# Optimization experiments

Hardware: AMD Instinct MI355X
Metric: run time of the kernel (lower is better)

## Reference

```python
import jax, jax.numpy as jnp
import numpy as np

EPS = 1e-6
N_HEAD = 16

def alibi_slopes(n_head):
    # standard ALiBi geometric slopes for power-of-2 head counts
    start = 2.0 ** (-8.0 / n_head)
    return (start ** np.arange(1, n_head + 1)).astype(np.float32)

def rsig(x):
    # rational sigmoid sigma(x) = 0.5 * (x / (|x| + 1) + 1)
    return 0.5 * (x / (jnp.abs(x) + 1.0) + 1.0)

def mr_norm(x, w):
    # RationalMR: x / (mean(|x|) + eps) * weight
    return x / (jnp.mean(jnp.abs(x), axis=-1, keepdims=True) + EPS) * w


def setup_inputs() -> dict:
    key = jax.random.key(0)
    ks = jax.random.split(key, 6)
    d_model, d_ffn = 1024, 4096
    B, T = 1, 2048
    x = jax.random.normal(ks[0], (B, T, d_model), dtype=jnp.float32)
    s = 0.02
    w_qkv = jax.random.normal(ks[1], (3 * d_model, d_model), dtype=jnp.float32) * s
    w_out = jax.random.normal(ks[2], (d_model, d_model), dtype=jnp.float32) * s
    w_merged = jax.random.normal(ks[3], (2 * d_ffn, d_model), dtype=jnp.float32) * s
    w3 = jax.random.normal(ks[4], (d_model, d_ffn), dtype=jnp.float32) * s
    norm1_w = jnp.ones((d_model,), dtype=jnp.float32)
    norm2_w = jnp.ones((d_model,), dtype=jnp.float32)
    return {"x": x, "w_qkv": w_qkv, "w_out": w_out, "w_merged": w_merged,
            "w3": w3, "norm1_w": norm1_w, "norm2_w": norm2_w}


def reference(x, w_qkv, w_out, w_merged, w3, norm1_w, norm2_w):
    B, T, C = x.shape
    H = N_HEAD
    D = C // H
    scale = 1.0 / jnp.sqrt(jnp.float32(D))

    # --- attention sub-block ---
    h = mr_norm(x, norm1_w)
    qkv = (h @ w_qkv.T).reshape(B, T, 3, H, D).transpose(2, 0, 3, 1, 4)  # [3,B,H,T,D]
    q, k, v = qkv[0], qkv[1], qkv[2]
    scores = jnp.einsum('bhtd,bhsd->bhts', q, k) * scale  # [B,H,T,T]
    pos = jnp.arange(T)
    rel = jnp.abs(pos[:, None] - pos[None, :]).astype(jnp.float32)
    slopes = jnp.asarray(alibi_slopes(H))
    scores = scores - rel[None, None] * slopes[None, :, None, None]
    causal = pos[None, :] > pos[:, None]  # mask j > i
    scores = jnp.where(causal[None, None], jnp.float32(-10000.0), scores)
    # rational softmax: sigma(s)^4 / (sum sigma(s)^4 + eps)
    p4 = rsig(scores) ** 4
    probs = p4 / (jnp.sum(p4, axis=-1, keepdims=True) + EPS)
    attn = jnp.einsum('bhts,bhsd->bhtd', probs, v)  # [B,H,T,D]
    attn = attn.transpose(0, 2, 1, 3).reshape(B, T, C)
    x = x + attn @ w_out.T

    # --- FFN sub-block (rational SwiGLU) ---
    h2 = mr_norm(x, norm2_w)
    merged = h2 @ w_merged.T
    gate, val = jnp.split(merged, 2, axis=-1)
    hidden = gate * rsig(gate) * val
    x = x + hidden @ w3.T
    return x
```

## Files before the change

### kernel.cpp

```cpp
#include <hip/hip_runtime.h>
#include <hip/hip_bf16.h>
#include <stdint.h>

typedef unsigned int u32;
typedef unsigned short u16;
typedef __attribute__((ext_vector_type(8))) short bf16x8;
typedef __attribute__((ext_vector_type(4))) float f32x4;

#define MFMA(a, b, c) __builtin_amdgcn_mfma_f32_16x16x32_bf16(a, b, c, 0, 0, 0)

__device__ __forceinline__ u16 f2bf(float f) {
  u32 u = __float_as_uint(f);
  return (u16)((u + 0x7FFFu + ((u >> 16) & 1u)) >> 16);
}
__device__ __forceinline__ float bf2f(u16 h) {
  return __uint_as_float(((u32)h) << 16);
}
__device__ __forceinline__ float rsig_fast(float sc) {
  return 0.5f + 0.5f * sc * __builtin_amdgcn_rcpf(fabsf(sc) + 1.f);
}
__device__ __forceinline__ void async16(void* lds, const void* g) {
  __builtin_amdgcn_global_load_lds((const __attribute__((address_space(1))) u32*)g,
                                   (__attribute__((address_space(3))) u32*)lds, 16, 0, 0);
}

__global__ __launch_bounds__(256) void to_bf16_all(const float* __restrict__ s0, u16* __restrict__ d0,
                                                   const float* __restrict__ s1, u16* __restrict__ d1,
                                                   const float* __restrict__ s2, u16* __restrict__ d2,
                                                   const float* __restrict__ s3, u16* __restrict__ d3) {
  int b = blockIdx.x;
  const float* src; u16* dst;
  if (b < 1536)      { src = s0; dst = d0; }
  else if (b < 2048) { src = s1; dst = d1; b -= 1536; }
  else if (b < 6144) { src = s2; dst = d2; b -= 2048; }
  else               { src = s3; dst = d3; b -= 6144; }
  const size_t i = (size_t)b * 256 + threadIdx.x;
  const float4 a = ((const float4*)src)[2 * i];
  const float4 c = ((const float4*)src)[2 * i + 1];
  ushort4 o0, o1;
  o0.x = f2bf(a.x); o0.y = f2bf(a.y); o0.z = f2bf(a.z); o0.w = f2bf(a.w);
  o1.x = f2bf(c.x); o1.y = f2bf(c.y); o1.z = f2bf(c.z); o1.w = f2bf(c.w);
  ((ushort4*)dst)[2 * i] = o0;
  ((ushort4*)dst)[2 * i + 1] = o1;
}

__global__ __launch_bounds__(256) void mrnorm(const float* __restrict__ x,
                                              const float* __restrict__ wg,
                                              u16* __restrict__ out) {
  const int row = blockIdx.x;
  const int tid = threadIdx.x;
  const float4 v = ((const float4*)(x + (size_t)row * 1024))[tid];
  float s = fabsf(v.x) + fabsf(v.y) + fabsf(v.z) + fabsf(v.w);
#pragma unroll
  for (int off = 1; off < 64; off <<= 1) s += __shfl_xor(s, off);
  __shared__ float red[4];
  if ((tid & 63) == 0) red[tid >> 6] = s;
  __syncthreads();
  const float inv = 1.f / ((red[0] + red[1] + red[2] + red[3]) * (1.f / 1024.f) + 1e-6f);
  const float4 g = ((const float4*)wg)[tid];
  ushort4 o;
  o.x = f2bf(v.x * inv * g.x);
  o.y = f2bf(v.y * inv * g.y);
  o.z = f2bf(v.z * inv * g.z);
  o.w = f2bf(v.w * inv * g.w);
  ((ushort4*)out)[(size_t)row * 256 + tid] = o;
}

__global__ __launch_bounds__(256) void wout_reduce_norm(const u16* __restrict__ part,
                                                        const float* __restrict__ x,
                                                        const float* __restrict__ wg,
                                                        float* __restrict__ x1,
                                                        u16* __restrict__ h2) {
  const int row = blockIdx.x;
  const int tid = threadIdx.x;
  const size_t base = (size_t)row * 1024 + tid * 4;
  float4 a = *(const float4*)(x + base);
#pragma unroll
  for (int c = 0; c < 4; ++c) {
    const ushort4 p = *(const ushort4*)(part + (size_t)c * 2097152 + base);
    a.x += bf2f(p.x); a.y += bf2f(p.y); a.z += bf2f(p.z); a.w += bf2f(p.w);
  }
  *(float4*)(x1 + base) = a;
  float s = fabsf(a.x) + fabsf(a.y) + fabsf(a.z) + fabsf(a.w);
#pragma unroll
  for (int off = 1; off < 64; off <<= 1) s += __shfl_xor(s, off);
  __shared__ float red[4];
  if ((tid & 63) == 0) red[tid >> 6] = s;
  __syncthreads();
  const float inv = 1.f / ((red[0] + red[1] + red[2] + red[3]) * (1.f / 1024.f) + 1e-6f);
  const float4 g = ((const float4*)wg)[tid];
  ushort4 o;
  o.x = f2bf(a.x * inv * g.x);
  o.y = f2bf(a.y * inv * g.y);
  o.z = f2bf(a.z * inv * g.z);
  o.w = f2bf(a.w * inv * g.w);
  ((ushort4*)h2)[(size_t)row * 256 + tid] = o;
}

template <int EPI, bool DBUF>
__global__ __launch_bounds__(256) void gemm_bt(const u16* __restrict__ A, int lda,
                                               const u16* __restrict__ B, int ldb,
                                               void* __restrict__ C,
                                               const float* __restrict__ resid,
                                               int M, int N, int K) {
  __shared__ __align__(16) u16 As[(DBUF ? 2 : 1) * 128 * 64];
  __shared__ __align__(16) u16 Bs[(DBUF ? 2 : 1) * 128 * 64];
  const int tid = threadIdx.x;
  const int lane = tid & 63;
  const int w = tid >> 6;
  const int wr = (w >> 1) << 6;
  const int wc = (w & 1) << 6;
  const int nbn = N >> 7;
  const int m0 = (blockIdx.x / nbn) << 7;
  const int n0 = (blockIdx.x % nbn) << 7;
  const int l15 = lane & 15;
  const int lhi = lane >> 4;
  A += (size_t)blockIdx.y * K;
  B += (size_t)blockIdx.y * K;

  f32x4 acc[4][4] = {};

  auto stage = [&](int buf, int k0) {
#pragma unroll
    for (int p = 0; p < 4; ++p) {
      const int c = p * 256 + tid;
      const int row = c >> 3;
      const int cb = (c & 7) << 4;
      const int src = cb ^ ((row & 7) << 4);
      async16((char*)As + buf * 16384 + c * 16,
              (const char*)A + ((size_t)(m0 + row) * lda + k0) * 2 + src);
      async16((char*)Bs + buf * 16384 + c * 16,
              (const char*)B + ((size_t)(n0 + row) * ldb + k0) * 2 + src);
    }
  };
  auto compute = [&](int buf) {
#pragma unroll
    for (int kk = 0; kk < 2; ++kk) {
      bf16x8 af[4], bfr[4];
#pragma unroll
      for (int m = 0; m < 4; ++m) {
        const int row = wr + (m << 4) + l15;
        const int off = row * 128 + (((kk << 6) + (lhi << 4)) ^ ((row & 7) << 4));
        af[m] = *(const bf16x8*)((const char*)As + buf * 16384 + off);
      }
#pragma unroll
      for (int n = 0; n < 4; ++n) {
        const int row = wc + (n << 4) + l15;
        const int off = row * 128 + (((kk << 6) + (lhi << 4)) ^ ((row & 7) << 4));
        bfr[n] = *(const bf16x8*)((const char*)Bs + buf * 16384 + off);
      }
#pragma unroll
      for (int m = 0; m < 4; ++m)
#pragma unroll
        for (int n = 0; n < 4; ++n)
          acc[m][n] = MFMA(af[m], bfr[n], acc[m][n]);
    }
  };

  if (DBUF) {
    stage(0, 0);
    __syncthreads();
    int cur = 0;
    for (int k0 = 0; k0 < K; k0 += 64) {
      if (k0 + 64 < K) stage(cur ^ 1, k0 + 64);
      compute(cur);
      __syncthreads();
      cur ^= 1;
    }
  } else {
    for (int k0 = 0; k0 < K; k0 += 64) {
      stage(0, k0);
      __syncthreads();
      compute(0);
      __syncthreads();
    }
  }

  u16* Cp = (u16*)C + (size_t)blockIdx.y * M * N;
#pragma unroll
  for (int m = 0; m < 4; ++m) {
#pragma unroll
    for (int n = 0; n < 4; ++n) {
      const int col = n0 + wc + (n << 4) + l15;
#pragma unroll
      for (int r = 0; r < 4; ++r) {
        const int row = m0 + wr + (m << 4) + (lhi << 2) + r;
        const float v = acc[m][n][r];
        if (EPI == 0) {
          Cp[(size_t)row * N + col] = f2bf(v);
        } else {
          const size_t idx = (size_t)row * N + col;
          ((float*)C)[idx] = resid[idx] + v;
        }
      }
    }
  }
}

__global__ __launch_bounds__(256) void gemm_ffn1(const u16* __restrict__ A,
                                                 const u16* __restrict__ B,
                                                 u16* __restrict__ hid) {
  __shared__ __align__(16) u16 As[2][128 * 64];
  __shared__ __align__(16) u16 Bg[2][64 * 64];
  __shared__ __align__(16) u16 Bv[2][64 * 64];
  const int tid = threadIdx.x;
  const int lane = tid & 63;
  const int w = tid >> 6;
  const int wr = (w >> 1) << 6;
  const int wc = (w & 1) << 5;
  const int m0 = (blockIdx.x >> 6) << 7;
  const int n0 = (blockIdx.x & 63) << 6;
  const int l15 = lane & 15;
  const int lhi = lane >> 4;

  f32x4 ag[4][2] = {};
  f32x4 av[4][2] = {};

  auto stage = [&](int buf, int k0) {
#pragma unroll
    for (int p = 0; p < 4; ++p) {
      const int c = p * 256 + tid;
      const int row = c >> 3;
      const int cb = (c & 7) << 4;
      const int src = cb ^ ((row & 7) << 4);
      async16((char*)As[buf] + c * 16,
              (const char*)A + ((size_t)(m0 + row) * 1024 + k0) * 2 + src);
    }
#pragma unroll
    for (int p = 0; p < 2; ++p) {
      const int c = p * 256 + tid;
      const int row = c >> 3;
      const int cb = (c & 7) << 4;
      const int src = cb ^ ((row & 7) << 4);
      async16((char*)Bg[buf] + c * 16,
              (const char*)B + ((size_t)(n0 + row) * 1024 + k0) * 2 + src);
      async16((char*)Bv[buf] + c * 16,
              (const char*)B + ((size_t)(4096 + n0 + row) * 1024 + k0) * 2 + src);
    }
  };
  auto compute = [&](int buf) {
#pragma unroll
    for (int kk = 0; kk < 2; ++kk) {
      bf16x8 af[4], bgf[2], bvf[2];
#pragma unroll
      for (int m = 0; m < 4; ++m) {
        const int row = wr + (m << 4) + l15;
        const int off = row * 128 + (((kk << 6) + (lhi << 4)) ^ ((row & 7) << 4));
        af[m] = *(const bf16x8*)((const char*)As[buf] + off);
      }
#pragma unroll
      for (int n = 0; n < 2; ++n) {
        const int row = wc + (n << 4) + l15;
        const int off = row * 128 + (((kk << 6) + (lhi << 4)) ^ ((row & 7) << 4));
        bgf[n] = *(const bf16x8*)((const char*)Bg[buf] + off);
        bvf[n] = *(const bf16x8*)((const char*)Bv[buf] + off);
      }
#pragma unroll
      for (int m = 0; m < 4; ++m)
#pragma unroll
        for (int n = 0; n < 2; ++n) {
          ag[m][n] = MFMA(af[m], bgf[n], ag[m][n]);
          av[m][n] = MFMA(af[m], bvf[n], av[m][n]);
        }
    }
  };

  stage(0, 0);
  __syncthreads();
  int cur = 0;
  for (int k0 = 0; k0 < 1024; k0 += 64) {
    if (k0 + 64 < 1024) stage(cur ^ 1, k0 + 64);
    compute(cur);
    __syncthreads();
    cur ^= 1;
  }

#pragma unroll
  for (int m = 0; m < 4; ++m) {
#pragma unroll
    for (int n = 0; n < 2; ++n) {
      const int col = n0 + wc + (n << 4) + l15;
#pragma unroll
      for (int r = 0; r < 4; ++r) {
        const int row = m0 + wr + (m << 4) + (lhi << 2) + r;
        const float g = ag[m][n][r];
        const float v = av[m][n][r];
        hid[(size_t)row * 4096 + col] = f2bf(g * rsig_fast(g) * v);
      }
    }
  }
}

template <int NC, bool BF16OUT>
__global__ __launch_bounds__(256) void splitk_reduce(const u16* __restrict__ part,
                                                     size_t cstride,
                                                     const float* __restrict__ resid,
                                                     void* __restrict__ out) {
  const size_t i = ((size_t)blockIdx.x * 256 + threadIdx.x) * 8;
  float acc[8];
  if constexpr (BF16OUT) {
#pragma unroll
    for (int j = 0; j < 8; ++j) acc[j] = 0.f;
  } else {
    const float4 r0 = *(const float4*)(resid + i);
    const float4 r1 = *(const float4*)(resid + i + 4);
    acc[0] = r0.x; acc[1] = r0.y; acc[2] = r0.z; acc[3] = r0.w;
    acc[4] = r1.x; acc[5] = r1.y; acc[6] = r1.z; acc[7] = r1.w;
  }
#pragma unroll
  for (int c = 0; c < NC; ++c) {
    const uint4 p = *(const uint4*)(part + (size_t)c * cstride + i);
    const u16* ps = (const u16*)&p;
#pragma unroll
    for (int j = 0; j < 8; ++j) acc[j] += bf2f(ps[j]);
  }
  if constexpr (BF16OUT) {
    u16 ob[8];
#pragma unroll
    for (int j = 0; j < 8; ++j) ob[j] = f2bf(acc[j]);
    *(uint4*)((u16*)out + i) = *(const uint4*)ob;
  } else {
    float4 o0 = {acc[0], acc[1], acc[2], acc[3]};
    float4 o1 = {acc[4], acc[5], acc[6], acc[7]};
    *(float4*)((float*)out + i) = o0;
    *(float4*)((float*)out + i + 4) = o1;
  }
}

__global__ __launch_bounds__(256) void transpose_v(const u16* __restrict__ qkv,
                                                   u16* __restrict__ vt) {
  __shared__ __align__(16) u16 tile[64][72];
  const int head = blockIdx.x >> 5;
  const int t0 = (blockIdx.x & 31) << 6;
  const int tid = threadIdx.x;
  const int row = tid >> 2;
  const int cb = (tid & 3) << 4;
  const u16* src = qkv + (size_t)(t0 + row) * 3072 + 2048 + head * 64 + cb;
  *(uint4*)&tile[row][cb] = *(const uint4*)src;
  *(uint4*)&tile[row][cb + 8] = *(const uint4*)(src + 8);
  __syncthreads();
  u16 buf[16];
#pragma unroll
  for (int j = 0; j < 16; ++j) buf[j] = tile[cb + j][row];
  u16* dst = vt + (size_t)(head * 64 + row) * 2048 + t0 + cb;
  *(uint4*)dst = *(const uint4*)&buf[0];
  *(uint4*)(dst + 8) = *(const uint4*)&buf[8];
}

__global__ __launch_bounds__(512) void attn_part(const u16* __restrict__ qkv,
                                                 const u16* __restrict__ vt,
                                                 u16* __restrict__ pnum,
                                                 float* __restrict__ pden) {
  const int id = blockIdx.x;
  const int head = id & 15;
  const int rem = id >> 4;
  int qb2, c;
  if (rem < 4)       { qb2 = 4 + rem;                          c = 0; }
  else if (rem < 12) { const int t = rem - 4;  qb2 = 8 + (t >> 1);  c = t & 1; }
  else if (rem < 24) { const int t = rem - 12; qb2 = 12 + t / 3;    c = t % 3; }
  else               { const int t = rem - 24; qb2 = ((t & 3) << 2) + 3 - (t >> 2); c = qb2 >> 2; }
  const int a2 = qb2 >> 2, b2 = qb2 & 3;
  const int slot = head * 40 + ((a2 * (a2 + 1)) << 1) + b2 * (a2 + 1) + c;

  __shared__ __align__(16) u16 Ks[2][64 * 64];
  __shared__ __align__(16) u16 Vs[2][64 * 64];
  __shared__ __align__(16) u16 QP[8][16 * 64];
  const int tid = threadIdx.x;
  const int lane = tid & 63;
  const int w = tid >> 6;
  const int l15 = lane & 15;
  const int lhi = lane >> 4;
  const int qbase = qb2 << 7;
  const float slope = exp2f(-0.5f * (float)(head + 1));

  auto stageKV = [&](int buf, int s0) {
    const int row = tid >> 3;
    const int cb = (tid & 7) << 4;
    const int src = cb ^ ((row & 7) << 4);
    async16((char*)Ks[buf] + tid * 16,
            (const char*)qkv + ((size_t)(s0 + row) * 3072 + 1024 + head * 64) * 2 + src);
    async16((char*)Vs[buf] + tid * 16,
            (const char*)vt + ((size_t)(head * 64 + row) * 2048 + s0) * 2 + src);
  };

  const int sfirst = c << 9;
  const int smax = min(qbase + 64, sfirst + 448);
#pragma unroll
  for (int p = 0; p < 2; ++p) {
    const int cc = p * 512 + tid;
    const int row = cc >> 3;
    const int cb = (cc & 7) << 4;
    const int src = cb ^ ((row & 7) << 4);
    async16((char*)QP + cc * 16,
            (const char*)qkv + ((size_t)(qbase + row) * 3072 + head * 64) * 2 + src);
  }
  stageKV(0, sfirst);
  __syncthreads();

  bf16x8 qf[2];
#pragma unroll
  for (int kk = 0; kk < 2; ++kk) {
    const int row = (w << 4) + l15;
    const int off = row * 128 + (((kk << 6) + (lhi << 4)) ^ ((row & 7) << 4));
    qf[kk] = *(const bf16x8*)((const char*)QP + off);
  }

  f32x4 oacc[4] = {};
  float rs[4] = {0.f, 0.f, 0.f, 0.f};
  u16* pw = (u16*)QP[w];
  int cur = 0;

  for (int s0 = sfirst; s0 <= smax; s0 += 64) {
    if (s0 + 64 <= smax) stageKV(cur ^ 1, s0 + 64);
    const char* Kc = (const char*)Ks[cur];
    const char* Vc = (const char*)Vs[cur];

    bf16x8 kf[4][2];
#pragma unroll
    for (int bb = 0; bb < 4; ++bb)
#pragma unroll
      for (int kk = 0; kk < 2; ++kk) {
        const int row = (bb << 4) + l15;
        const int off = row * 128 + (((kk << 6) + (lhi << 4)) ^ ((row & 7) << 4));
        kf[bb][kk] = *(const bf16x8*)(Kc + off);
      }
    f32x4 sa[4];
    __builtin_amdgcn_s_setprio(1);
#pragma unroll
    for (int bb = 0; bb < 4; ++bb) {
      f32x4 z = {0.f, 0.f, 0.f, 0.f};
      z = MFMA(qf[0], kf[bb][0], z);
      sa[bb] = MFMA(qf[1], kf[bb][1], z);
    }
    __builtin_amdgcn_s_setprio(0);
#pragma unroll
    for (int bb = 0; bb < 4; ++bb) {
      const int s_abs = s0 + (bb << 4) + l15;
#pragma unroll
      for (int r = 0; r < 4; ++r) {
        const int prow = (lhi << 2) + r;
        const int q_abs = qbase + (w << 4) + prow;
        float p4 = 0.f;
        if (s_abs <= q_abs) {
          const float sc = sa[bb][r] * 0.125f - slope * (float)(q_abs - s_abs);
          const float t = rsig_fast(sc);
          const float t2 = t * t;
          p4 = t2 * t2;
        }
        rs[r] += p4;
        const int pcol2 = ((bb << 4) + l15) << 1;
        const int poff = prow * 128 + (pcol2 ^ ((prow & 7) << 4));
        *(u16*)((char*)pw + poff) = f2bf(p4);
      }
    }
    bf16x8 pf[2];
#pragma unroll
    for (int kk = 0; kk < 2; ++kk) {
      const int row = l15;
      const int off = row * 128 + (((kk << 6) + (lhi << 4)) ^ ((row & 7) << 4));
      pf[kk] = *(const bf16x8*)((const char*)pw + off);
    }
    __builtin_amdgcn_s_setprio(1);
#pragma unroll
    for (int db = 0; db < 4; ++db) {
#pragma unroll
      for (int kk = 0; kk < 2; ++kk) {
        const int row = (db << 4) + l15;
        const int off = row * 128 + (((kk << 6) + (lhi << 4)) ^ ((row & 7) << 4));
        const bf16x8 vf = *(const bf16x8*)(Vc + off);
        oacc[db] = MFMA(pf[kk], vf, oacc[db]);
      }
    }
    __builtin_amdgcn_s_setprio(0);
    __syncthreads();
    cur ^= 1;
  }

#pragma unroll
  for (int r = 0; r < 4; ++r) {
    float v = rs[r];
    v += __shfl_xor(v, 1);
    v += __shfl_xor(v, 2);
    v += __shfl_xor(v, 4);
    v += __shfl_xor(v, 8);
    rs[r] = v;
  }
  if (l15 == 0) {
#pragma unroll
    for (int r = 0; r < 4; ++r)
      pden[(size_t)slot * 128 + (w << 4) + (lhi << 2) + r] = rs[r];
  }
  __syncthreads();
#pragma unroll
  for (int db = 0; db < 4; ++db)
#pragma unroll
    for (int r = 0; r < 4; ++r)
      pw[((lhi << 2) + r) * 64 + (db << 4) + l15] = f2bf(oacc[db][r]);
  __syncthreads();
  {
    const int row = lane >> 2;
    const int cb = (lane & 3) << 4;
    const u16* s = pw + row * 64 + cb;
    const uint4 d0 = *(const uint4*)s;
    const uint4 d1 = *(const uint4*)(s + 8);
    u16* dst = pnum + (size_t)slot * 8192 + ((w << 4) + row) * 64 + cb;
    *(uint4*)dst = d0;
    *(uint4*)(dst + 8) = d1;
  }
}

__global__ __launch_bounds__(256) void attn_merge(const u16* __restrict__ pnum,
                                                  const float* __restrict__ pden,
                                                  u16* __restrict__ out) {
  const int head = blockIdx.x >> 5;
  const int qb = blockIdx.x & 31;
  const int qb2 = qb >> 1;
  const int a2 = qb >> 3;
  const int nc = a2 + 1;
  const int slot0 = head * 40 + ((a2 * (a2 + 1)) << 1) + (qb2 & 3) * (a2 + 1);
  const int tid = threadIdx.x;
  const int row = tid >> 2;
  const int c0 = (tid & 3) << 4;
  const int rr = ((qb & 1) << 6) + row;

  float acc[16] = {};
  float den = 0.f;
  for (int ci = 0; ci < nc; ++ci) {
    const int slot = slot0 + ci;
    den += pden[(size_t)slot * 128 + rr];
    const u16* np = pnum + (size_t)slot * 8192 + rr * 64 + c0;
    const uint4 n0 = *(const uint4*)np;
    const uint4 n1 = *(const uint4*)(np + 8);
    const u16* ns0 = (const u16*)&n0;
    const u16* ns1 = (const u16*)&n1;
#pragma unroll
    for (int j = 0; j < 8; ++j) {
      acc[j] += bf2f(ns0[j]);
      acc[8 + j] += bf2f(ns1[j]);
    }
  }
  const float inv = 1.f / (den + 1e-6f);
  u16 ob[16];
#pragma unroll
  for (int j = 0; j < 16; ++j) ob[j] = f2bf(acc[j] * inv);
  u16* dst = out + (size_t)((qb << 6) + row) * 1024 + head * 64 + c0;
  *(uint4*)dst = *(const uint4*)&ob[0];
  *(uint4*)(dst + 8) = *(const uint4*)&ob[8];
}

extern "C" void kernel_launch(void* const* d_in, const int* in_sizes, int n_in,
                              void* d_out, int out_size, void* d_ws, size_t ws_size,
                              hipStream_t stream) {
  const float* x     = (const float*)d_in[0];
  const float* wqkv  = (const float*)d_in[1];
  const float* wout  = (const float*)d_in[2];
  const float* wmer  = (const float*)d_in[3];
  const float* w3    = (const float*)d_in[4];
  const float* n1w   = (const float*)d_in[5];
  const float* n2w   = (const float*)d_in[6];
  char* ws = (char*)d_ws;

  u16*   WQKV = (u16*)(ws + 0);
  u16*   WOUT = (u16*)(ws + 6291456);
  u16*   WMER = (u16*)(ws + 8388608);
  u16*   W3B  = (u16*)(ws + 25165824);
  u16*   H    = (u16*)(ws + 33554432);
  u16*   QKV  = (u16*)(ws + 37748736);
  u16*   VT   = (u16*)(ws + 50331648);
  u16*   PNUM = (u16*)(ws + 54525952);
  float* PDEN = (float*)(ws + 65011712);
  u16*   ATTN = (u16*)(ws + 65536000);
  u16*   WOP  = (u16*)(ws + 37748736);
  float* X1   = (float*)(ws + 54525952);
  u16*   H2   = (u16*)(ws + 33554432);
  u16*   HID  = (u16*)(ws + 37748736);
  u16*   W3P  = (u16*)(ws + 62914560);

  to_bf16_all<<<8192, 256, 0, stream>>>(wqkv, WQKV, wout, WOUT, wmer, WMER, w3, W3B);

  mrnorm<<<2048, 256, 0, stream>>>(x, n1w, H);
  gemm_bt<0, true><<<16 * 24, 256, 0, stream>>>(H, 1024, WQKV, 1024, QKV, nullptr,
                                                2048, 3072, 1024);
  transpose_v<<<512, 256, 0, stream>>>(QKV, VT);
  attn_part<<<640, 512, 0, stream>>>(QKV, VT, PNUM, PDEN);
  attn_merge<<<512, 256, 0, stream>>>(PNUM, PDEN, ATTN);
  gemm_bt<0, true><<<dim3(16 * 8, 4), 256, 0, stream>>>(ATTN, 1024, WOUT, 1024, WOP,
                                                        nullptr, 2048, 1024, 256);
  wout_reduce_norm<<<2048, 256, 0, stream>>>(WOP, x, n2w, X1, H2);

  gemm_ffn1<<<1024, 256, 0, stream>>>(H2, WMER, HID);
  gemm_bt<0, true><<<dim3(16 * 8, 4), 256, 0, stream>>>(HID, 4096, W3B, 4096, W3P,
                                                        nullptr, 2048, 1024, 1024);
  splitk_reduce<4, false><<<1024, 256, 0, stream>>>(W3P, 2097152, X1, (float*)d_out);
}
```

Before: 165.4 us.

## Prefetch two K-tiles ahead with explicit vmcnt waits in GEMM loops

Replaces the single-stage prefetch loop with a two-deep async prefetch in both gemm_bt and the SwiGLU GEMM. Stage k+2 is issued after compute of step k, and partial s_waitcnt vmcnt waits let only the older tile's loads drain before each barrier. The goal is to keep more global-to-LDS loads in flight and hide memory latency behind MFMA work. It adds an extra barrier per step, forces double buffering on every gemm_bt instantiation (more LDS, possibly lower occupancy), and relies on the hand-chosen vmcnt count matching the number of loads issued per stage.

```diff
diff --git a/kernel.cpp b/kernel.cpp
--- a/kernel.cpp
+++ b/kernel.cpp
@@ -8,6 +8,11 @@
 typedef __attribute__((ext_vector_type(4))) float f32x4;
 
 #define MFMA(a, b, c) __builtin_amdgcn_mfma_f32_16x16x32_bf16(a, b, c, 0, 0, 0)
+
+#define BARRIER_PINNED() do { __builtin_amdgcn_s_barrier(); \
+                              __builtin_amdgcn_sched_barrier(0); } while (0)
+#define WAITV8() asm volatile("s_waitcnt vmcnt(8)" ::: "memory")
+#define WAITV0() asm volatile("s_waitcnt vmcnt(0)" ::: "memory")
 
 __device__ __forceinline__ u16 f2bf(float f) {
   u32 u = __float_as_uint(f);
@@ -103,8 +108,8 @@
                                                void* __restrict__ C,
                                                const float* __restrict__ resid,
                                                int M, int N, int K) {
-  __shared__ __align__(16) u16 As[(DBUF ? 2 : 1) * 128 * 64];
-  __shared__ __align__(16) u16 Bs[(DBUF ? 2 : 1) * 128 * 64];
+  __shared__ __align__(16) u16 As[2 * 128 * 64];
+  __shared__ __align__(16) u16 Bs[2 * 128 * 64];
   const int tid = threadIdx.x;
   const int lane = tid & 63;
   const int w = tid >> 6;
@@ -157,23 +162,23 @@
     }
   };
 
-  if (DBUF) {
-    stage(0, 0);
-    __syncthreads();
-    int cur = 0;
-    for (int k0 = 0; k0 < K; k0 += 64) {
-      if (k0 + 64 < K) stage(cur ^ 1, k0 + 64);
-      compute(cur);
-      __syncthreads();
-      cur ^= 1;
-    }
-  } else {
-    for (int k0 = 0; k0 < K; k0 += 64) {
-      stage(0, k0);
-      __syncthreads();
-      compute(0);
-      __syncthreads();
-    }
+  const int nsteps = K >> 6;
+  stage(0, 0);
+  stage(1, 64);
+  WAITV8();
+  BARRIER_PINNED();
+  int cur = 0;
+  for (int step = 0; step < nsteps; ++step) {
+    compute(cur);
+    BARRIER_PINNED();
+    if (step + 2 < nsteps) {
+      stage(cur, (step + 2) << 6);
+      WAITV8();
+    } else if (step + 1 < nsteps) {
+      WAITV0();
+    }
+    BARRIER_PINNED();
+    cur ^= 1;
   }
 
   u16* Cp = (u16*)C + (size_t)blockIdx.y * M * N;
@@ -266,12 +271,20 @@
   };
 
   stage(0, 0);
-  __syncthreads();
+  stage(1, 64);
+  WAITV8();
+  BARRIER_PINNED();
   int cur = 0;
-  for (int k0 = 0; k0 < 1024; k0 += 64) {
-    if (k0 + 64 < 1024) stage(cur ^ 1, k0 + 64);
+  for (int step = 0; step < 16; ++step) {
     compute(cur);
-    __syncthreads();
+    BARRIER_PINNED();
+    if (step + 2 < 16) {
+      stage(cur, (step + 2) << 6);
+      WAITV8();
+    } else if (step + 1 < 16) {
+      WAITV0();
+    }
+    BARRIER_PINNED();
     cur ^= 1;
   }
 
```

Measured after the change: 169.5 us. 2.4% more time.
